# Kernel tuning notes

Measured on AMD Instinct MI355X. Metric: run time of the kernel, lower is better.

The kernel has to match this reference:

```python
import jax, jax.numpy as jnp
import numpy as np

N = 40000          # nodes
E = 320000         # edges
IN_DIM = 16
H = 64             # num_hidden
EDGE_DIM = 8
NUM_FILTERS = 2
SCALE = 3
T = 4              # num_layers (time steps)
DC = EDGE_DIM * NUM_FILTERS   # edge_dim_cat = 16
HC = H + DC                   # concat(h, efeat_p) dim
S1 = SCALE - 1


def setup_inputs() -> dict:
    key = jax.random.key(0)
    ks = jax.random.split(key, 24)
    def nrm(k, shape, fan):
        return jax.random.normal(k, shape, dtype=jnp.float32) / np.float32(np.sqrt(fan))
    return {
        "inputs": jax.random.normal(ks[0], (N, IN_DIM), dtype=jnp.float32),
        "e_feats": jax.random.normal(ks[1], (E, EDGE_DIM, T), dtype=jnp.float32),
        "rain0": jax.random.uniform(ks[2], (N, T), dtype=jnp.float32),
        "src": jax.random.randint(ks[3], (E,), 0, N),
        "dst": jax.random.randint(ks[4], (E,), 0, N),
        # embedding (no bias)
        "W_emb": nrm(ks[5], (IN_DIM, H), IN_DIM),
        # ST_EIConvSPGRAD (IN) layers, one per scale step: edge MLP split into per-source terms
        "Win_hs": nrm(ks[6], (S1, H, H), 2 * H + EDGE_DIM + 1),
        "Win_hd": nrm(ks[7], (S1, H, H), 2 * H + EDGE_DIM + 1),
        "Win_e": nrm(ks[8], (S1, EDGE_DIM, H), 2 * H + EDGE_DIM + 1),
        "Win_r": nrm(ks[9], (S1, H), 2 * H + EDGE_DIM + 1),
        # ST_EIConvProp (PROP) layers (edge-feature propagation, out_on=False)
        "Wp_hs": nrm(ks[10], (S1, H, DC), 2 * H + DC + 1),
        "Wp_hd": nrm(ks[11], (S1, H, DC), 2 * H + DC + 1),
        "Wp_e": nrm(ks[12], (S1, DC, DC), 2 * H + DC + 1),
        "Wp_r": nrm(ks[13], (S1, DC), 2 * H + DC + 1),
        # ST_EIConvProp OUT layer (out_on=True) on concatenated node features
        "Wo_hs": nrm(ks[14], (HC, H), 2 * HC + EDGE_DIM + 1),
        "Wo_hd": nrm(ks[15], (HC, H), 2 * HC + EDGE_DIM + 1),
        "Wo_e": nrm(ks[16], (EDGE_DIM, H), 2 * HC + EDGE_DIM + 1),
        "Wo_r": nrm(ks[17], (H,), 2 * HC + EDGE_DIM + 1),
        "W_rain": nrm(ks[18], (H,), H),
    }


def reference(inputs, e_feats, rain0, src, dst,
              W_emb, Win_hs, Win_hd, Win_e, Win_r,
              Wp_hs, Wp_hd, Wp_e, Wp_r,
              Wo_hs, Wo_hd, Wo_e, Wo_r, W_rain):
    relu = jax.nn.relu
    agg = lambda m: jax.ops.segment_sum(m, dst, num_segments=N)

    def in_layer(s, h, ef, rain):
        # per-edge message: MLP over [h_src, h_dst, efeat, rain_src], split matmuls avoid concat
        m = relu(h[src] @ Win_hs[s] + h[dst] @ Win_hd[s]
                 + ef @ Win_e[s] + rain[src, None] * Win_r[s][None, :])
        return relu(agg(m))                      # [N, H]

    def prop_layer(s, h, ef, rain):
        # ef is edge-level [E, DC] on first call, node-level [N, DC] thereafter (gather at src)
        ef_e = ef if ef.shape[0] == E else ef[src]
        m = relu(h[src] @ Wp_hs[s] + h[dst] @ Wp_hd[s]
                 + ef_e @ Wp_e[s] + rain[src, None] * Wp_r[s][None, :])
        return agg(m)                            # [N, DC]

    def out_layer(h_out, ef, rain):
        m = relu(h_out[src] @ Wo_hs + h_out[dst] @ Wo_hd
                 + ef @ Wo_e + rain[src, None] * Wo_r[None, :])
        h_new = relu(agg(m))                     # [N, H]
        rain_out = h_new @ W_rain                # [N]
        return rain_out, h_new

    def step(h, ef_t, rain_t, first):
        for s in range(S1):
            h = in_layer(s, h, ef_t, rain_t)
        ef_exp = jnp.tile(ef_t, (1, NUM_FILTERS))        # [E, DC]
        p = prop_layer(0, h, ef_exp, rain_t)
        # faithful quirk: first time step re-applies PROP[0] (range starts at 0);
        # later steps start at 1
        rng = range(S1) if first else range(1, S1)
        for s in rng:
            p = prop_layer(s, h, p, rain_t)
        h_out = jnp.concatenate([h, p], axis=1)          # [N, HC]
        rain_m, h = out_layer(h_out, ef_t, rain_t)
        return rain_m, h

    h = inputs @ W_emb                                   # [N, H]
    rains = []
    for t in range(T):
        rain_m, h = step(h, e_feats[:, :, t], rain0[:, t], first=(t == 0))
        rains.append(rain_m)
    return jnp.stack(rains, axis=1)                      # [N, T]
```

## Files before the change

kernel.cpp:

```cpp
#include <hip/hip_runtime.h>

#define NN 40000
#define NE 320000
#define TT 4
#define SCAN_CHUNK 1024
#define NBLK_SCAN ((NN + SCAN_CHUNK - 1) / SCAN_CHUNK)

typedef unsigned short u16;

__device__ __forceinline__ float bcastf(float v, int k) {
    return __builtin_bit_cast(float, __builtin_amdgcn_readlane(__builtin_bit_cast(int, v), k));
}
__device__ __forceinline__ int bcasti(int v, int k) {
    return __builtin_amdgcn_readlane(v, k);
}
__device__ __forceinline__ float b2f(u16 u) {
    return __builtin_bit_cast(float, (unsigned)u << 16);
}
__device__ __forceinline__ u16 f2b(float f) {
    unsigned x = __builtin_bit_cast(unsigned, f);
    unsigned r = x + 0x7fffu + ((x >> 16) & 1u);
    return (u16)(r >> 16);
}
__device__ __forceinline__ float lo16(unsigned u) {
    return __builtin_bit_cast(float, u << 16);
}
__device__ __forceinline__ float hi16(unsigned u) {
    return __builtin_bit_cast(float, u & 0xffff0000u);
}

__global__ void emb_kernel(const float* __restrict__ x, const float* __restrict__ W,
                           float* __restrict__ h) {
    int i = blockIdx.x * blockDim.x + threadIdx.x;
    if (i >= NN * 64) return;
    int n = i >> 6, j = i & 63;
    float acc = 0.f;
#pragma unroll
    for (int k = 0; k < 16; ++k) acc = fmaf(x[n * 16 + k], W[k * 64 + j], acc);
    h[i] = acc;
}

__global__ void wfold_kernel(const float* __restrict__ We, float* __restrict__ Wf) {
    int i = threadIdx.x;
    if (i < 128) Wf[i] = We[i] + We[i + 128];
}

__global__ void hist_kernel(const int* __restrict__ dst, int* __restrict__ deg) {
    int e = blockIdx.x * blockDim.x + threadIdx.x;
    if (e < NE) atomicAdd(&deg[dst[e]], 1);
}

__global__ void scan1_kernel(const int* __restrict__ deg, int* __restrict__ bsum) {
    __shared__ int sdata[256];
    int b = blockIdx.x, t = threadIdx.x;
    int base = b * SCAN_CHUNK;
    int sum = 0;
    for (int i = t; i < SCAN_CHUNK; i += 256) {
        int idx = base + i;
        sum += (idx < NN) ? deg[idx] : 0;
    }
    sdata[t] = sum;
    __syncthreads();
    for (int off = 128; off > 0; off >>= 1) {
        if (t < off) sdata[t] += sdata[t + off];
        __syncthreads();
    }
    if (t == 0) bsum[b] = sdata[0];
}

__global__ void scan2_kernel(const int* __restrict__ bsum, int* __restrict__ boff,
                             int* __restrict__ rowptr) {
    if (threadIdx.x == 0) {
        int acc = 0;
        for (int i = 0; i < NBLK_SCAN; ++i) {
            boff[i] = acc;
            acc += bsum[i];
        }
        rowptr[NN] = NE;
    }
}

__global__ void scan3_kernel(const int* __restrict__ deg, const int* __restrict__ boff,
                             int* __restrict__ rowptr, int* __restrict__ cursor) {
    __shared__ int ss[256];
    int b = blockIdx.x, t = threadIdx.x;
    int base = b * SCAN_CHUNK + t * 4;
    int v[4], s = 0;
#pragma unroll
    for (int q = 0; q < 4; ++q) {
        int idx = base + q;
        v[q] = (idx < NN) ? deg[idx] : 0;
        s += v[q];
    }
    ss[t] = s;
    __syncthreads();
    for (int off = 1; off < 256; off <<= 1) {
        int add = (t >= off) ? ss[t - off] : 0;
        __syncthreads();
        ss[t] += add;
        __syncthreads();
    }
    int excl = boff[b] + ss[t] - s;
#pragma unroll
    for (int q = 0; q < 4; ++q) {
        int idx = base + q;
        if (idx < NN) {
            rowptr[idx] = excl;
            cursor[idx] = excl;
        }
        excl += v[q];
    }
}

__global__ void scatter_kernel(const int* __restrict__ src, const int* __restrict__ dst,
                               int* __restrict__ cursor, int* __restrict__ perm,
                               int* __restrict__ srcp) {
    int e = blockIdx.x * blockDim.x + threadIdx.x;
    if (e >= NE) return;
    int d = dst[e];
    int pos = atomicAdd(&cursor[d], 1);
    perm[pos] = e;
    srcp[pos] = src[e];
}

__global__ void efperm_all_kernel(const float* __restrict__ ef, const int* __restrict__ perm,
                                  u16* __restrict__ out) {
    int pos = blockIdx.x * blockDim.x + threadIdx.x;
    if (pos >= NE) return;
    int e = perm[pos];
    const float4* e4 = reinterpret_cast<const float4*>(ef) + (size_t)e * 8;
#pragma unroll
    for (int k = 0; k < 8; ++k) {
        float4 v = e4[k];
        out[0 * (size_t)NE * 8 + pos * 8 + k] = f2b(v.x);
        out[1 * (size_t)NE * 8 + pos * 8 + k] = f2b(v.y);
        out[2 * (size_t)NE * 8 + pos * 8 + k] = f2b(v.z);
        out[3 * (size_t)NE * 8 + pos * 8 + k] = f2b(v.w);
    }
}

__global__ void efperm_one_kernel(const float* __restrict__ ef, const int* __restrict__ perm,
                                  int t, u16* __restrict__ out) {
    int i = blockIdx.x * blockDim.x + threadIdx.x;
    if (i >= NE * 8) return;
    int pos = i >> 3, k = i & 7;
    int e = perm[pos];
    out[i] = f2b(ef[((size_t)e * 8 + k) * 4 + t]);
}

__global__ __launch_bounds__(256) void node_ab_kernel(
    const float* __restrict__ X1, int relu1,
    const float* __restrict__ X2, int d2,
    const float* __restrict__ Whs, const float* __restrict__ Whd,
    const float* __restrict__ rain, const float* __restrict__ Wr,
    u16* __restrict__ A, u16* __restrict__ B) {
    extern __shared__ float sW[];
    const int dtot = 64 + d2;
    float* sWs = sW;
    float* sWd = sW + (dtot << 6);
    for (int i = threadIdx.x; i < (dtot << 6); i += 256) {
        sWs[i] = Whs[i];
        sWd[i] = Whd[i];
    }
    __syncthreads();
    const int lane = threadIdx.x & 63;
    const int wid = (blockIdx.x << 2) + (threadIdx.x >> 6);
    const int n0 = wid << 3;
    const float wr = Wr[lane];
    float xv[8], aa[8], bb[8];
#pragma unroll
    for (int p = 0; p < 8; ++p) {
        float x = __builtin_nontemporal_load(&X1[(n0 + p) * 64 + lane]);
        xv[p] = relu1 ? fmaxf(x, 0.f) : x;
        aa[p] = rain[(n0 + p) * TT] * wr;
        bb[p] = 0.f;
    }
#pragma unroll 16
    for (int k = 0; k < 64; ++k) {
        float ws = sWs[(k << 6) + lane];
        float wd = sWd[(k << 6) + lane];
#pragma unroll
        for (int p = 0; p < 8; ++p) {
            float xk = bcastf(xv[p], k);
            aa[p] = fmaf(xk, ws, aa[p]);
            bb[p] = fmaf(xk, wd, bb[p]);
        }
    }
    if (d2) {
#pragma unroll
        for (int p = 0; p < 8; ++p) xv[p] = X2[(n0 + p) * 16 + (lane & 15)];
#pragma unroll
        for (int k = 0; k < 16; ++k) {
            float ws = sWs[((64 + k) << 6) + lane];
            float wd = sWd[((64 + k) << 6) + lane];
#pragma unroll
            for (int p = 0; p < 8; ++p) {
                float xk = bcastf(xv[p], k);
                aa[p] = fmaf(xk, ws, aa[p]);
                bb[p] = fmaf(xk, wd, bb[p]);
            }
        }
    }
#pragma unroll
    for (int p = 0; p < 8; ++p) {
        A[(n0 + p) * 64 + lane] = f2b(aa[p]);
        B[(n0 + p) * 64 + lane] = f2b(bb[p]);
    }
}

__global__ __launch_bounds__(256) void node_p_all(
    const float* __restrict__ X,
    const float* __restrict__ Whs, const float* __restrict__ Whd,
    const float* __restrict__ rain, const float* __restrict__ Wr,
    float* __restrict__ Ap0, float* __restrict__ Bp0,
    float* __restrict__ Ap1, float* __restrict__ Bp1) {
    __shared__ float sX[64 * 68];
    __shared__ float sW[4][1024];
    for (int i = threadIdx.x; i < 1024; i += 256) {
        sW[0][i] = Whs[i];
        sW[1][i] = Whd[i];
        sW[2][i] = Whs[1024 + i];
        sW[3][i] = Whd[1024 + i];
    }
    const int n0 = blockIdx.x << 6;
    for (int i = threadIdx.x; i < 1024; i += 256) {
        int row = i >> 4, col = (i & 15) << 2;
        const float4 v = *reinterpret_cast<const float4*>(&X[(n0 + row) * 64 + col]);
        float* d = &sX[row * 68 + col];
        d[0] = fmaxf(v.x, 0.f);
        d[1] = fmaxf(v.y, 0.f);
        d[2] = fmaxf(v.z, 0.f);
        d[3] = fmaxf(v.w, 0.f);
    }
    __syncthreads();
    const int j = threadIdx.x & 15;
    const int nl0 = threadIdx.x >> 4;
    const float wr0 = Wr[j], wr1 = Wr[16 + j];
    float a0[4], b0[4], a1[4], b1[4];
#pragma unroll
    for (int q = 0; q < 4; ++q) {
        float rn = rain[(n0 + nl0 + (q << 4)) * TT];
        a0[q] = rn * wr0;
        a1[q] = rn * wr1;
        b0[q] = 0.f;
        b1[q] = 0.f;
    }
#pragma unroll 4
    for (int k = 0; k < 64; ++k) {
        float wa0 = sW[0][(k << 4) + j], wb0 = sW[1][(k << 4) + j];
        float wa1 = sW[2][(k << 4) + j], wb1 = sW[3][(k << 4) + j];
#pragma unroll
        for (int q = 0; q < 4; ++q) {
            float x = sX[(nl0 + (q << 4)) * 68 + k];
            a0[q] = fmaf(x, wa0, a0[q]);
            b0[q] = fmaf(x, wb0, b0[q]);
            a1[q] = fmaf(x, wa1, a1[q]);
            b1[q] = fmaf(x, wb1, b1[q]);
        }
    }
#pragma unroll
    for (int q = 0; q < 4; ++q) {
        int n = n0 + nl0 + (q << 4);
        Ap0[n * 16 + j] = a0[q];
        Bp0[n * 16 + j] = b0[q];
        Ap1[n * 16 + j] = a1[q];
        Bp1[n * 16 + j] = b1[q];
    }
}

__global__ __launch_bounds__(256) void edge64_csr(
    const u16* __restrict__ A, const u16* __restrict__ B,
    const u16* __restrict__ efp, const float* __restrict__ We,
    const int* __restrict__ rowptr, const int* __restrict__ srcp,
    float* __restrict__ agg, const float* __restrict__ Wrain,
    float* __restrict__ out, int t) {
    const int lane = threadIdx.x & 63;
    const int n = (blockIdx.x << 2) + (threadIdx.x >> 6);
    const float w0 = We[lane], w1 = We[64 + lane];
    const float w2 = We[128 + lane], w3 = We[192 + lane];
    const float w4 = We[256 + lane], w5 = We[320 + lane];
    const float w6 = We[384 + lane], w7 = We[448 + lane];
    const int beg = rowptr[n], end = rowptr[n + 1];
    const int deg = end - beg;
    int sv = 0;
    if (beg + lane < NE) sv = srcp[beg + lane];
    const float b = b2f(__builtin_nontemporal_load(&B[(size_t)n * 64 + lane]));
    const uint4* ef4 = reinterpret_cast<const uint4*>(efp);
    float acc = 0.f;
    for (int k0 = 0; k0 < deg; k0 += 4) {
        u16 av[4];
        uint4 ev[4];
#pragma unroll
        for (int i = 0; i < 4; ++i) {
            int kk = k0 + i;
            if (kk > deg - 1) kk = deg - 1;
            int s = (kk < 64) ? bcasti(sv, kk) : srcp[beg + kk];
            av[i] = A[(size_t)s * 64 + lane];
            ev[i] = ef4[(size_t)(beg + kk)];
        }
#pragma unroll
        for (int i = 0; i < 4; ++i) {
            if (k0 + i < deg) {
                float m = b2f(av[i]) + b;
                m = fmaf(lo16(ev[i].x), w0, m);
                m = fmaf(hi16(ev[i].x), w1, m);
                m = fmaf(lo16(ev[i].y), w2, m);
                m = fmaf(hi16(ev[i].y), w3, m);
                m = fmaf(lo16(ev[i].z), w4, m);
                m = fmaf(hi16(ev[i].z), w5, m);
                m = fmaf(lo16(ev[i].w), w6, m);
                m = fmaf(hi16(ev[i].w), w7, m);
                acc += fmaxf(m, 0.f);
            }
        }
    }
    __builtin_nontemporal_store(acc, &agg[(size_t)n * 64 + lane]);
    if (out) {
        float r = fmaxf(acc, 0.f) * Wrain[lane];
#pragma unroll
        for (int off = 32; off > 0; off >>= 1) r += __shfl_down(r, off);
        if (lane == 0) out[n * TT + t] = r;
    }
}

__global__ __launch_bounds__(256) void edge16_csr(
    const float* __restrict__ G, const float* __restrict__ Bp,
    const u16* __restrict__ efp, const float* __restrict__ Wf, int has_ef,
    const float* __restrict__ ApN, const float* __restrict__ WeN,
    float* __restrict__ PeSN, int has_epi,
    const int* __restrict__ rowptr, const int* __restrict__ srcp,
    float* __restrict__ pout) {
    const int lane = threadIdx.x & 63;
    const int g = lane >> 4, j = lane & 15;
    float w[8];
    if (has_ef) {
#pragma unroll
        for (int k = 0; k < 8; ++k) w[k] = Wf[k * 16 + j];
    }
    const int wid = (blockIdx.x * 256 + threadIdx.x) >> 6;
    const int n = (wid << 2) + g;
    const int beg = rowptr[n], end = rowptr[n + 1];
    const float b = Bp[n * 16 + j];
    const uint4* ef4 = reinterpret_cast<const uint4*>(efp);
    float acc = 0.f;
    int s_nxt = (beg + 1 < end) ? srcp[beg + 1] : 0;
    float av = (beg < end) ? G[srcp[beg] * 16 + j] : 0.f;
    for (int pos = beg; pos < end; ++pos) {
        float avc = av;
        int s_nn = (pos + 2 < end) ? srcp[pos + 2] : 0;
        if (pos + 1 < end) av = G[s_nxt * 16 + j];
        s_nxt = s_nn;
        float m = avc + b;
        if (has_ef) {
            uint4 ev = ef4[(size_t)pos];
            m = fmaf(lo16(ev.x), w[0], m);
            m = fmaf(hi16(ev.x), w[1], m);
            m = fmaf(lo16(ev.y), w[2], m);
            m = fmaf(hi16(ev.y), w[3], m);
            m = fmaf(lo16(ev.z), w[4], m);
            m = fmaf(hi16(ev.z), w[5], m);
            m = fmaf(lo16(ev.w), w[6], m);
            m = fmaf(hi16(ev.w), w[7], m);
        }
        acc += fmaxf(m, 0.f);
    }
    if (pout) pout[n * 16 + j] = acc;
    if (has_epi) {
        float pe = ApN[n * 16 + j];
        const int gbase = lane & 48;
#pragma unroll
        for (int k = 0; k < 16; ++k) {
            float pk = __shfl(acc, gbase + k);
            pe = fmaf(pk, WeN[k * 16 + j], pe);
        }
        PeSN[n * 16 + j] = pe;
    }
}

extern "C" void kernel_launch(void* const* d_in, const int* in_sizes, int n_in,
                              void* d_out, int out_size, void* d_ws, size_t ws_size,
                              hipStream_t stream) {
    (void)in_sizes; (void)n_in; (void)out_size;
    const float* inputs = (const float*)d_in[0];
    const float* e_feats = (const float*)d_in[1];
    const float* rain0 = (const float*)d_in[2];
    const int* src = (const int*)d_in[3];
    const int* dst = (const int*)d_in[4];
    const float* W_emb = (const float*)d_in[5];
    const float* Win_hs = (const float*)d_in[6];
    const float* Win_hd = (const float*)d_in[7];
    const float* Win_e = (const float*)d_in[8];
    const float* Win_r = (const float*)d_in[9];
    const float* Wp_hs = (const float*)d_in[10];
    const float* Wp_hd = (const float*)d_in[11];
    const float* Wp_e = (const float*)d_in[12];
    const float* Wp_r = (const float*)d_in[13];
    const float* Wo_hs = (const float*)d_in[14];
    const float* Wo_hd = (const float*)d_in[15];
    const float* Wo_e = (const float*)d_in[16];
    const float* Wo_r = (const float*)d_in[17];
    const float* W_rain = (const float*)d_in[18];
    float* out = (float*)d_out;

    const size_t NF64 = (size_t)NN * 64;
    const size_t NF16 = (size_t)NN * 16;
    const size_t EF = (size_t)NE * 8;

    char* base = (char*)d_ws;
    auto alloc = [&](size_t bytes) -> char* {
        char* p = base;
        base += (bytes + 255) & ~(size_t)255;
        return p;
    };

    const size_t need_big = (4 * NF64 + 7 * NF16 + 128) * 4 + (2 * NF64 + 4 * EF) * 2 +
                            (2 * (size_t)NE + 3 * (size_t)NN + 200) * 4 + 64 * 256;
    const bool big = ws_size >= need_big;

    float *aggA, *aggB, *aggO, *hemb, *pbuf, *Ap0, *Bp0, *Ap1, *Bp1, *PeSa, *PeSb, *Wfold;
    u16 *A16, *B16, *efp16;
    if (big) {
        aggA = (float*)alloc(NF64 * 4);
        aggB = (float*)alloc(NF64 * 4);
        aggO = (float*)alloc(NF64 * 4);
        hemb = (float*)alloc(NF64 * 4);
        Ap0 = (float*)alloc(NF16 * 4);
        Bp0 = (float*)alloc(NF16 * 4);
        Ap1 = (float*)alloc(NF16 * 4);
        Bp1 = (float*)alloc(NF16 * 4);
        PeSa = (float*)alloc(NF16 * 4);
        PeSb = (float*)alloc(NF16 * 4);
        pbuf = (float*)alloc(NF16 * 4);
        A16 = (u16*)alloc(NF64 * 2);
        B16 = (u16*)alloc(NF64 * 2);
        efp16 = (u16*)alloc(4 * EF * 2);
        Wfold = (float*)alloc(128 * 4);
    } else {
        aggA = (float*)alloc(NF64 * 4);
        aggB = (float*)alloc(NF64 * 4);
        aggO = (float*)alloc(NF64 * 4);
        A16 = (u16*)alloc(NF64 * 2);
        B16 = (u16*)alloc(NF64 * 2);
        efp16 = (u16*)alloc(EF * 2);
        Wfold = (float*)alloc(128 * 4);
        hemb = aggO;
        Ap0 = aggA;
        Bp0 = aggA + NF16;
        Ap1 = aggA + 2 * NF16;
        Bp1 = aggA + 3 * NF16;
        PeSa = (float*)B16;
        PeSb = (float*)A16;
        pbuf = aggO;
    }
    int* srcp = (int*)alloc(NE * 4);
    int* perm = (int*)alloc(NE * 4);
    int* rowptr = (int*)alloc((NN + 1) * 4);
    int* deg = (int*)alloc(NN * 4);
    int* cursor = (int*)alloc(NN * 4);
    int* bsum = (int*)alloc(64 * 4);
    int* boff = (int*)alloc(64 * 4);

    hipMemsetAsync(deg, 0, NN * sizeof(int), stream);
    hist_kernel<<<(NE + 255) / 256, 256, 0, stream>>>(dst, deg);
    scan1_kernel<<<NBLK_SCAN, 256, 0, stream>>>(deg, bsum);
    scan2_kernel<<<1, 64, 0, stream>>>(bsum, boff, rowptr);
    scan3_kernel<<<NBLK_SCAN, 256, 0, stream>>>(deg, boff, rowptr, cursor);
    scatter_kernel<<<(NE + 255) / 256, 256, 0, stream>>>(src, dst, cursor, perm, srcp);
    if (big)
        efperm_all_kernel<<<(NE + 255) / 256, 256, 0, stream>>>(e_feats, perm, efp16);

    emb_kernel<<<(NN * 64 + 255) / 256, 256, 0, stream>>>(inputs, W_emb, hemb);
    wfold_kernel<<<1, 128, 0, stream>>>(Wp_e, Wfold);

    for (int t = 0; t < TT; ++t) {
        const float* rain = rain0 + t;
        const u16* eft = big ? (efp16 + (size_t)t * EF) : efp16;
        if (!big)
            efperm_one_kernel<<<(NE * 8 + 255) / 256, 256, 0, stream>>>(e_feats, perm, t, efp16);

        node_ab_kernel<<<1250, 256, 64 * 64 * 2 * sizeof(float), stream>>>(
            (t == 0) ? hemb : aggO, (t > 0) ? 1 : 0, nullptr, 0,
            Win_hs, Win_hd, rain, Win_r, A16, B16);
        edge64_csr<<<10000, 256, 0, stream>>>(A16, B16, eft, Win_e, rowptr, srcp, aggA,
                                              nullptr, nullptr, 0);

        node_ab_kernel<<<1250, 256, 64 * 64 * 2 * sizeof(float), stream>>>(
            aggA, 1, nullptr, 0, Win_hs + 4096, Win_hd + 4096, rain, Win_r + 64, A16, B16);
        edge64_csr<<<10000, 256, 0, stream>>>(A16, B16, eft, Win_e + 512, rowptr, srcp, aggB,
                                              nullptr, nullptr, 0);

        node_p_all<<<625, 256, 0, stream>>>(aggB, Wp_hs, Wp_hd, rain, Wp_r,
                                            Ap0, Bp0, Ap1, Bp1);

        if (t == 0) {
            edge16_csr<<<2500, 256, 0, stream>>>(Ap0, Bp0, eft, Wfold, 1,
                                                 Ap0, Wp_e, PeSa, 1,
                                                 rowptr, srcp, nullptr);
            edge16_csr<<<2500, 256, 0, stream>>>(PeSa, Bp0, nullptr, nullptr, 0,
                                                 Ap1, Wp_e + 256, PeSb, 1,
                                                 rowptr, srcp, nullptr);
            edge16_csr<<<2500, 256, 0, stream>>>(PeSb, Bp1, nullptr, nullptr, 0,
                                                 nullptr, nullptr, nullptr, 0,
                                                 rowptr, srcp, pbuf);
        } else {
            edge16_csr<<<2500, 256, 0, stream>>>(Ap0, Bp0, eft, Wfold, 1,
                                                 Ap1, Wp_e + 256, PeSa, 1,
                                                 rowptr, srcp, nullptr);
            edge16_csr<<<2500, 256, 0, stream>>>(PeSa, Bp1, nullptr, nullptr, 0,
                                                 nullptr, nullptr, nullptr, 0,
                                                 rowptr, srcp, pbuf);
        }

        node_ab_kernel<<<1250, 256, 80 * 64 * 2 * sizeof(float), stream>>>(
            aggB, 1, pbuf, 16, Wo_hs, Wo_hd, rain, Wo_r, A16, B16);
        edge64_csr<<<10000, 256, 0, stream>>>(A16, B16, eft, Wo_e, rowptr, srcp, aggO,
                                              W_rain, out, t);
    }
}
```

Before: 960.7 us.

## Fuse next-layer node GEMMs into edge aggregation kernels and store activations in bf16

Each edge CSR kernel now computes the following node-level projection in its epilogue. The second IN layer's A/B come from the first edge kernel, and the PROP Ap/Bp projections come from the second, which removes one node_ab launch and node_p_all per step along with their global round-trips. Aggregated node features are stored as bf16 instead of fp32 to halve node traffic. The cost is that every edge block loads 16–32KB of weights into shared memory, which may lower occupancy, and activations lose precision.

Result: slower. 1.055 ms (+9.8%).

```diff
diff --git a/kernel.cpp b/kernel.cpp
--- a/kernel.cpp
+++ b/kernel.cpp
@@ -30,14 +30,14 @@
 }
 
 __global__ void emb_kernel(const float* __restrict__ x, const float* __restrict__ W,
-                           float* __restrict__ h) {
+                           u16* __restrict__ h) {
     int i = blockIdx.x * blockDim.x + threadIdx.x;
     if (i >= NN * 64) return;
     int n = i >> 6, j = i & 63;
     float acc = 0.f;
 #pragma unroll
     for (int k = 0; k < 16; ++k) acc = fmaf(x[n * 16 + k], W[k * 64 + j], acc);
-    h[i] = acc;
+    h[i] = f2b(acc);
 }
 
 __global__ void wfold_kernel(const float* __restrict__ We, float* __restrict__ Wf) {
@@ -149,7 +149,7 @@
 }
 
 __global__ __launch_bounds__(256) void node_ab_kernel(
-    const float* __restrict__ X1, int relu1,
+    const u16* __restrict__ X1, int relu1,
     const float* __restrict__ X2, int d2,
     const float* __restrict__ Whs, const float* __restrict__ Whd,
     const float* __restrict__ rain, const float* __restrict__ Wr,
@@ -170,7 +170,7 @@
     float xv[8], aa[8], bb[8];
 #pragma unroll
     for (int p = 0; p < 8; ++p) {
-        float x = __builtin_nontemporal_load(&X1[(n0 + p) * 64 + lane]);
+        float x = b2f(__builtin_nontemporal_load(&X1[(size_t)(n0 + p) * 64 + lane]));
         xv[p] = relu1 ? fmaxf(x, 0.f) : x;
         aa[p] = rain[(n0 + p) * TT] * wr;
         bb[p] = 0.f;
@@ -203,77 +203,40 @@
     }
 #pragma unroll
     for (int p = 0; p < 8; ++p) {
-        A[(n0 + p) * 64 + lane] = f2b(aa[p]);
-        B[(n0 + p) * 64 + lane] = f2b(bb[p]);
-    }
-}
-
-__global__ __launch_bounds__(256) void node_p_all(
-    const float* __restrict__ X,
-    const float* __restrict__ Whs, const float* __restrict__ Whd,
-    const float* __restrict__ rain, const float* __restrict__ Wr,
-    float* __restrict__ Ap0, float* __restrict__ Bp0,
-    float* __restrict__ Ap1, float* __restrict__ Bp1) {
-    __shared__ float sX[64 * 68];
-    __shared__ float sW[4][1024];
-    for (int i = threadIdx.x; i < 1024; i += 256) {
-        sW[0][i] = Whs[i];
-        sW[1][i] = Whd[i];
-        sW[2][i] = Whs[1024 + i];
-        sW[3][i] = Whd[1024 + i];
-    }
-    const int n0 = blockIdx.x << 6;
-    for (int i = threadIdx.x; i < 1024; i += 256) {
-        int row = i >> 4, col = (i & 15) << 2;
-        const float4 v = *reinterpret_cast<const float4*>(&X[(n0 + row) * 64 + col]);
-        float* d = &sX[row * 68 + col];
-        d[0] = fmaxf(v.x, 0.f);
-        d[1] = fmaxf(v.y, 0.f);
-        d[2] = fmaxf(v.z, 0.f);
-        d[3] = fmaxf(v.w, 0.f);
-    }
-    __syncthreads();
-    const int j = threadIdx.x & 15;
-    const int nl0 = threadIdx.x >> 4;
-    const float wr0 = Wr[j], wr1 = Wr[16 + j];
-    float a0[4], b0[4], a1[4], b1[4];
-#pragma unroll
-    for (int q = 0; q < 4; ++q) {
-        float rn = rain[(n0 + nl0 + (q << 4)) * TT];
-        a0[q] = rn * wr0;
-        a1[q] = rn * wr1;
-        b0[q] = 0.f;
-        b1[q] = 0.f;
-    }
-#pragma unroll 4
-    for (int k = 0; k < 64; ++k) {
-        float wa0 = sW[0][(k << 4) + j], wb0 = sW[1][(k << 4) + j];
-        float wa1 = sW[2][(k << 4) + j], wb1 = sW[3][(k << 4) + j];
-#pragma unroll
-        for (int q = 0; q < 4; ++q) {
-            float x = sX[(nl0 + (q << 4)) * 68 + k];
-            a0[q] = fmaf(x, wa0, a0[q]);
-            b0[q] = fmaf(x, wb0, b0[q]);
-            a1[q] = fmaf(x, wa1, a1[q]);
-            b1[q] = fmaf(x, wb1, b1[q]);
-        }
-    }
-#pragma unroll
-    for (int q = 0; q < 4; ++q) {
-        int n = n0 + nl0 + (q << 4);
-        Ap0[n * 16 + j] = a0[q];
-        Bp0[n * 16 + j] = b0[q];
-        Ap1[n * 16 + j] = a1[q];
-        Bp1[n * 16 + j] = b1[q];
-    }
-}
-
+        A[(size_t)(n0 + p) * 64 + lane] = f2b(aa[p]);
+        B[(size_t)(n0 + p) * 64 + lane] = f2b(bb[p]);
+    }
+}
+
+template <int MODE>
 __global__ __launch_bounds__(256) void edge64_csr(
     const u16* __restrict__ A, const u16* __restrict__ B,
     const u16* __restrict__ efp, const float* __restrict__ We,
     const int* __restrict__ rowptr, const int* __restrict__ srcp,
-    float* __restrict__ agg, const float* __restrict__ Wrain,
-    float* __restrict__ out, int t) {
+    const float* __restrict__ rain,
+    const float* __restrict__ WhsN, const float* __restrict__ WhdN,
+    const float* __restrict__ WrN, u16* __restrict__ Aout, u16* __restrict__ Bout,
+    const float* __restrict__ Wp_r,
+    float* __restrict__ Ap0, float* __restrict__ Bp0,
+    float* __restrict__ Ap1, float* __restrict__ Bp1,
+    u16* __restrict__ agg,
+    const float* __restrict__ Wrain, float* __restrict__ out, int t) {
+    extern __shared__ float sW[];
+    if (MODE == 1) {
+        for (int i = threadIdx.x; i < 4096; i += 256) {
+            sW[i] = WhsN[i];
+            sW[4096 + i] = WhdN[i];
+        }
+        __syncthreads();
+    } else if (MODE == 2) {
+        for (int i = threadIdx.x; i < 1024; i += 256) {
+            sW[i] = WhsN[i];
+            sW[1024 + i] = WhdN[i];
+            sW[2048 + i] = WhsN[1024 + i];
+            sW[3072 + i] = WhdN[1024 + i];
+        }
+        __syncthreads();
+    }
     const int lane = threadIdx.x & 63;
     const int n = (blockIdx.x << 2) + (threadIdx.x >> 6);
     const float w0 = We[lane], w1 = We[64 + lane];
@@ -314,12 +277,38 @@
             }
         }
     }
-    __builtin_nontemporal_store(acc, &agg[(size_t)n * 64 + lane]);
-    if (out) {
+    if (MODE == 0) {
+        __builtin_nontemporal_store(f2b(acc), &agg[(size_t)n * 64 + lane]);
         float r = fmaxf(acc, 0.f) * Wrain[lane];
 #pragma unroll
         for (int off = 32; off > 0; off >>= 1) r += __shfl_down(r, off);
         if (lane == 0) out[n * TT + t] = r;
+    } else if (MODE == 1) {
+        float xr = fmaxf(acc, 0.f);
+        float a = rain[n * TT] * WrN[lane];
+        float bb = 0.f;
+#pragma unroll 16
+        for (int k = 0; k < 64; ++k) {
+            float xk = bcastf(xr, k);
+            a = fmaf(xk, sW[(k << 6) + lane], a);
+            bb = fmaf(xk, sW[4096 + (k << 6) + lane], bb);
+        }
+        Aout[(size_t)n * 64 + lane] = f2b(a);
+        Bout[(size_t)n * 64 + lane] = f2b(bb);
+    } else {
+        __builtin_nontemporal_store(f2b(acc), &agg[(size_t)n * 64 + lane]);
+        float xr = fmaxf(acc, 0.f);
+        const int q = lane >> 4, j = lane & 15;
+        float rn = rain[n * TT];
+        float v = (q == 0) ? rn * Wp_r[j] : ((q == 2) ? rn * Wp_r[16 + j] : 0.f);
+        const float* wq = sW + (q << 10);
+#pragma unroll 16
+        for (int k = 0; k < 64; ++k) {
+            float xk = bcastf(xr, k);
+            v = fmaf(xk, wq[(k << 4) + j], v);
+        }
+        float* d = (q & 2) ? ((q & 1) ? Bp1 : Ap1) : ((q & 1) ? Bp0 : Ap0);
+        d[n * 16 + j] = v;
     }
 }
 
@@ -413,45 +402,27 @@
         return p;
     };
 
-    const size_t need_big = (4 * NF64 + 7 * NF16 + 128) * 4 + (2 * NF64 + 4 * EF) * 2 +
-                            (2 * (size_t)NE + 3 * (size_t)NN + 200) * 4 + 64 * 256;
-    const bool big = ws_size >= need_big;
-
-    float *aggA, *aggB, *aggO, *hemb, *pbuf, *Ap0, *Bp0, *Ap1, *Bp1, *PeSa, *PeSb, *Wfold;
-    u16 *A16, *B16, *efp16;
-    if (big) {
-        aggA = (float*)alloc(NF64 * 4);
-        aggB = (float*)alloc(NF64 * 4);
-        aggO = (float*)alloc(NF64 * 4);
-        hemb = (float*)alloc(NF64 * 4);
-        Ap0 = (float*)alloc(NF16 * 4);
-        Bp0 = (float*)alloc(NF16 * 4);
-        Ap1 = (float*)alloc(NF16 * 4);
-        Bp1 = (float*)alloc(NF16 * 4);
-        PeSa = (float*)alloc(NF16 * 4);
-        PeSb = (float*)alloc(NF16 * 4);
-        pbuf = (float*)alloc(NF16 * 4);
-        A16 = (u16*)alloc(NF64 * 2);
-        B16 = (u16*)alloc(NF64 * 2);
-        efp16 = (u16*)alloc(4 * EF * 2);
-        Wfold = (float*)alloc(128 * 4);
-    } else {
-        aggA = (float*)alloc(NF64 * 4);
-        aggB = (float*)alloc(NF64 * 4);
-        aggO = (float*)alloc(NF64 * 4);
-        A16 = (u16*)alloc(NF64 * 2);
-        B16 = (u16*)alloc(NF64 * 2);
-        efp16 = (u16*)alloc(EF * 2);
-        Wfold = (float*)alloc(128 * 4);
-        hemb = aggO;
-        Ap0 = aggA;
-        Bp0 = aggA + NF16;
-        Ap1 = aggA + 2 * NF16;
-        Bp1 = aggA + 3 * NF16;
-        PeSa = (float*)B16;
-        PeSb = (float*)A16;
-        pbuf = aggO;
-    }
+    const size_t fixed = 6 * NF64 * 2 + 7 * NF16 * 4 +
+                         (2 * (size_t)NE + 3 * (size_t)NN + 200) * 4 + 64 * 256;
+    const bool big = ws_size >= fixed + 4 * EF * 2;
+
+    u16 *A16a, *B16a, *A16b, *B16b, *aggB16, *aggO16, *efp16;
+    float *Ap0, *Bp0, *Ap1, *Bp1, *PeSa, *PeSb, *pbuf, *Wfold;
+    A16a = (u16*)alloc(NF64 * 2);
+    B16a = (u16*)alloc(NF64 * 2);
+    A16b = (u16*)alloc(NF64 * 2);
+    B16b = (u16*)alloc(NF64 * 2);
+    aggB16 = (u16*)alloc(NF64 * 2);
+    aggO16 = (u16*)alloc(NF64 * 2);
+    Ap0 = (float*)alloc(NF16 * 4);
+    Bp0 = (float*)alloc(NF16 * 4);
+    Ap1 = (float*)alloc(NF16 * 4);
+    Bp1 = (float*)alloc(NF16 * 4);
+    PeSa = (float*)alloc(NF16 * 4);
+    PeSb = (float*)alloc(NF16 * 4);
+    pbuf = (float*)alloc(NF16 * 4);
+    Wfold = (float*)alloc(128 * 4);
+    efp16 = (u16*)alloc((big ? 4 * EF : EF) * 2);
     int* srcp = (int*)alloc(NE * 4);
     int* perm = (int*)alloc(NE * 4);
     int* rowptr = (int*)alloc((NN + 1) * 4);
@@ -459,6 +430,7 @@
     int* cursor = (int*)alloc(NN * 4);
     int* bsum = (int*)alloc(64 * 4);
     int* boff = (int*)alloc(64 * 4);
+    u16* hemb = aggO16;
 
     hipMemsetAsync(deg, 0, NN * sizeof(int), stream);
     hist_kernel<<<(NE + 255) / 256, 256, 0, stream>>>(dst, deg);
@@ -479,18 +451,19 @@
             efperm_one_kernel<<<(NE * 8 + 255) / 256, 256, 0, stream>>>(e_feats, perm, t, efp16);
 
         node_ab_kernel<<<1250, 256, 64 * 64 * 2 * sizeof(float), stream>>>(
-            (t == 0) ? hemb : aggO, (t > 0) ? 1 : 0, nullptr, 0,
-            Win_hs, Win_hd, rain, Win_r, A16, B16);
-        edge64_csr<<<10000, 256, 0, stream>>>(A16, B16, eft, Win_e, rowptr, srcp, aggA,
-                                              nullptr, nullptr, 0);
-
-        node_ab_kernel<<<1250, 256, 64 * 64 * 2 * sizeof(float), stream>>>(
-            aggA, 1, nullptr, 0, Win_hs + 4096, Win_hd + 4096, rain, Win_r + 64, A16, B16);
-        edge64_csr<<<10000, 256, 0, stream>>>(A16, B16, eft, Win_e + 512, rowptr, srcp, aggB,
-                                              nullptr, nullptr, 0);
-
-        node_p_all<<<625, 256, 0, stream>>>(aggB, Wp_hs, Wp_hd, rain, Wp_r,
-                                            Ap0, Bp0, Ap1, Bp1);
+            aggO16, (t > 0) ? 1 : 0, nullptr, 0,
+            Win_hs, Win_hd, rain, Win_r, A16a, B16a);
+        edge64_csr<1><<<10000, 256, 32768, stream>>>(
+            A16a, B16a, eft, Win_e, rowptr, srcp, rain,
+            Win_hs + 4096, Win_hd + 4096, Win_r + 64, A16b, B16b,
+            nullptr, nullptr, nullptr, nullptr, nullptr, nullptr,
+            nullptr, nullptr, 0);
+
+        edge64_csr<2><<<10000, 256, 16384, stream>>>(
+            A16b, B16b, eft, Win_e + 512, rowptr, srcp, rain,
+            Wp_hs, Wp_hd, nullptr, nullptr, nullptr,
+            Wp_r, Ap0, Bp0, Ap1, Bp1, aggB16,
+            nullptr, nullptr, 0);
 
         if (t == 0) {
             edge16_csr<<<2500, 256, 0, stream>>>(Ap0, Bp0, eft, Wfold, 1,
@@ -512,8 +485,11 @@
         }
 
         node_ab_kernel<<<1250, 256, 80 * 64 * 2 * sizeof(float), stream>>>(
-            aggB, 1, pbuf, 16, Wo_hs, Wo_hd, rain, Wo_r, A16, B16);
-        edge64_csr<<<10000, 256, 0, stream>>>(A16, B16, eft, Wo_e, rowptr, srcp, aggO,
-                                              W_rain, out, t);
-    }
-}
+            aggB16, 1, pbuf, 16, Wo_hs, Wo_hd, rain, Wo_r, A16a, B16a);
+        edge64_csr<0><<<10000, 256, 0, stream>>>(
+            A16a, B16a, eft, Wo_e, rowptr, srcp, rain,
+            nullptr, nullptr, nullptr, nullptr, nullptr,
+            nullptr, nullptr, nullptr, nullptr, nullptr, aggO16,
+            W_rain, out, t);
+    }
+}
```
